# Optimization experiments

Hardware: AMD Instinct MI355X
Metric: run time of the kernel (lower is better)

## Reference

```python
import jax, jax.numpy as jnp
import numpy as np

N_NODES = 100000
N_EDGES = 1600000
IN_DIM = 64
HID = 64
EDGE_DIM = 1
NUM_GRAPHS = 1000
SCALE = 0.05


def setup_inputs() -> dict:
    key = jax.random.key(0)
    ks = jax.random.split(key, 20)
    x = jax.random.normal(ks[0], (N_NODES, IN_DIM), dtype=jnp.float32)
    edge_index = jax.random.randint(ks[1], (2, N_EDGES), 0, N_NODES, dtype=jnp.int64)
    edge_attr = jax.random.normal(ks[2], (N_EDGES, EDGE_DIM), dtype=jnp.float32)
    batch = jnp.sort(jax.random.randint(ks[3], (N_NODES,), 0, NUM_GRAPHS, dtype=jnp.int64))
    p = lambda k, shp: SCALE * jax.random.normal(k, shp, dtype=jnp.float32)
    return {
        "x": x, "edge_index": edge_index, "edge_attr": edge_attr, "batch": batch,
        # conv1 MLP + edge lin
        "W1a": p(ks[4], (IN_DIM, HID)), "b1a": p(ks[5], (HID,)),
        "W1b": p(ks[6], (HID, HID)), "b1b": p(ks[7], (HID,)),
        "We1": p(ks[8], (EDGE_DIM, IN_DIM)), "be1": p(ks[9], (IN_DIM,)),
        # conv2 MLP + edge lin
        "W2a": p(ks[10], (HID, HID)), "b2a": p(ks[11], (HID,)),
        "W2b": p(ks[12], (HID, HID)), "b2b": p(ks[13], (HID,)),
        "We2": p(ks[14], (EDGE_DIM, HID)), "be2": p(ks[15], (HID,)),
        # classifier
        "Wc1": p(ks[16], (HID, HID)), "bc1": p(ks[17], (HID,)),
        "Wc2": p(ks[18], (HID, 1)), "bc2": p(ks[19], (1,)),
    }


def _gine(x, src, dst, e_proj, Wa, ba, Wb, bb):
    # message: ReLU(x_src + projected edge feature); scatter-sum to target
    msg = jax.nn.relu(x[src] + e_proj)                      # [E, D]
    agg = jax.ops.segment_sum(msg, dst, num_segments=x.shape[0])
    h = x + agg                                             # eps = 0 (default)
    return jax.nn.relu(h @ Wa + ba) @ Wb + bb               # GIN MLP


def reference(x, edge_index, edge_attr, batch,
              W1a, b1a, W1b, b1b, We1, be1,
              W2a, b2a, W2b, b2b, We2, be2,
              Wc1, bc1, Wc2, bc2):
    src, dst = edge_index[0], edge_index[1]
    h = _gine(x, src, dst, edge_attr @ We1 + be1, W1a, b1a, W1b, b1b)
    h = jax.nn.relu(h)  # dropout is identity in eval mode
    h = _gine(h, src, dst, edge_attr @ We2 + be2, W2a, b2a, W2b, b2b)
    h = jax.nn.relu(h)
    # global mean pool over graphs
    sums = jax.ops.segment_sum(h, batch, num_segments=NUM_GRAPHS)
    cnts = jax.ops.segment_sum(jnp.ones((h.shape[0], 1), h.dtype), batch, num_segments=NUM_GRAPHS)
    pooled = sums / jnp.maximum(cnts, 1.0)                  # [G, HID]
    return jax.nn.relu(pooled @ Wc1 + bc1) @ Wc2 + bc2      # [G, 1]
```

## Files before the change

kernel.cpp:

```cpp
#include <hip/hip_runtime.h>

#define N_NODES    100000
#define N_EDGES    1600000
#define DIM        64
#define NUM_GRAPHS 1000
#define CONV_BLK   3125
#define PAD        72

#define SLICES     512
#define SLICE_E    3125
#define NBUCK      782
#define CAP4       3072

typedef __attribute__((ext_vector_type(8))) short bf16x8;
typedef __attribute__((ext_vector_type(4))) float f32x4;

__device__ __forceinline__ unsigned short f2bf(float f) {
    unsigned int b = __float_as_uint(f);
    b += 0x7FFFu + ((b >> 16) & 1u);
    return (unsigned short)(b >> 16);
}

__device__ __forceinline__ float4 ntload_f4(const float* p) {
    f32x4 v = __builtin_nontemporal_load((const f32x4*)p);
    return make_float4(v.x, v.y, v.z, v.w);
}

__global__ __launch_bounds__(256) void prep(
    const int* __restrict__ ei, const float* __restrict__ x,
    int* __restrict__ hist, int* __restrict__ bucketTotal,
    unsigned short* __restrict__ x16)
{
    __shared__ int lh[NBUCK];
    int blk = blockIdx.x, t = threadIdx.x;
    if (blk < SLICES) {
        for (int i = t; i < NBUCK; i += 256) lh[i] = 0;
        __syncthreads();
        const int* dsts = ei + N_EDGES + blk * SLICE_E;
        for (int k = t; k < SLICE_E; k += 256)
            atomicAdd(&lh[dsts[k] >> 7], 1);
        __syncthreads();
        for (int i = t; i < NBUCK; i += 256) {
            int h = lh[i];
            hist[blk * NBUCK + i] = h;
            if (h) atomicAdd(&bucketTotal[i], h);
        }
    } else {
        int tt = (blk - SLICES) * 256 + t;
        if (tt < N_NODES * DIM / 8) {
            int base = tt * 8;
            float4 f0 = ntload_f4(x + base);
            float4 f1 = ntload_f4(x + base + 4);
            uint4 o;
            o.x = (unsigned)f2bf(f0.x) | ((unsigned)f2bf(f0.y) << 16);
            o.y = (unsigned)f2bf(f0.z) | ((unsigned)f2bf(f0.w) << 16);
            o.z = (unsigned)f2bf(f1.x) | ((unsigned)f2bf(f1.y) << 16);
            o.w = (unsigned)f2bf(f1.z) | ((unsigned)f2bf(f1.w) << 16);
            *(uint4*)(x16 + base) = o;
        }
    }
}

__global__ __launch_bounds__(1024) void csr_c2a(
    const int* __restrict__ bucketTotal, int* __restrict__ bucketStart)
{
    __shared__ int sc[1024];
    int t = threadIdx.x;
    int v = (t < NBUCK) ? bucketTotal[t] : 0;
    sc[t] = v;
    __syncthreads();
    for (int o = 1; o < 1024; o <<= 1) {
        int u = (t >= o) ? sc[t - o] : 0;
        __syncthreads();
        sc[t] += u;
        __syncthreads();
    }
    if (t < NBUCK) bucketStart[t] = sc[t] - v;
    if (t == NBUCK - 1) bucketStart[NBUCK] = sc[t];
}

__global__ __launch_bounds__(512) void csr_c2b(
    const int* __restrict__ hist, const int* __restrict__ bucketStart,
    int* __restrict__ off)
{
    __shared__ int sc[512];
    int b = blockIdx.x, t = threadIdx.x;
    int v = hist[t * NBUCK + b];
    sc[t] = v;
    __syncthreads();
    for (int o = 1; o < 512; o <<= 1) {
        int u = (t >= o) ? sc[t - o] : 0;
        __syncthreads();
        sc[t] += u;
        __syncthreads();
    }
    off[b * SLICES + t] = bucketStart[b] + sc[t] - v;
}

__global__ __launch_bounds__(256) void csr_c3(
    const int* __restrict__ ei, const float* __restrict__ ea,
    const int* __restrict__ hist, const int* __restrict__ off,
    int2* __restrict__ tmp)
{
    __shared__ int2 staging[SLICE_E];
    __shared__ int  lstart[NBUCK + 1];
    __shared__ int  garr[NBUCK];
    __shared__ int  lcur[NBUCK];
    __shared__ unsigned short barr[SLICE_E];
    __shared__ int  part[256];

    int s = blockIdx.x, t = threadIdx.x;

    int h[4];
    int mysum = 0;
    #pragma unroll
    for (int j = 0; j < 4; ++j) {
        int b = 4 * t + j;
        h[j] = (b < NBUCK) ? hist[s * NBUCK + b] : 0;
        mysum += h[j];
    }
    part[t] = mysum;
    for (int i = t; i < NBUCK; i += 256) {
        garr[i] = off[i * SLICES + s];
        lcur[i] = 0;
    }
    __syncthreads();
    for (int o = 1; o < 256; o <<= 1) {
        int u = (t >= o) ? part[t - o] : 0;
        __syncthreads();
        part[t] += u;
        __syncthreads();
    }
    int run = part[t] - mysum;
    #pragma unroll
    for (int j = 0; j < 4; ++j) {
        int b = 4 * t + j;
        if (b < NBUCK) lstart[b] = run;
        run += h[j];
    }
    if (t == 0) lstart[NBUCK] = SLICE_E;
    __syncthreads();

    #pragma unroll
    for (int j = 0; j < 4; ++j) {
        int b = 4 * t + j;
        if (b < NBUCK)
            for (int i = lstart[b]; i < lstart[b + 1]; ++i)
                barr[i] = (unsigned short)b;
    }
    __syncthreads();

    for (int k = t; k < SLICE_E; k += 256) {
        int e   = s * SLICE_E + k;
        int src = ei[e];
        int dst = ei[N_EDGES + e];
        float a = ea[e];
        int b   = dst >> 7;
        int p   = lstart[b] + atomicAdd(&lcur[b], 1);
        staging[p] = make_int2(((dst & 127) << 17) | src, __float_as_int(a));
    }
    __syncthreads();

    for (int i = t; i < SLICE_E; i += 256) {
        int b = barr[i];
        tmp[garr[b] + (i - lstart[b])] = staging[i];
    }
}

__global__ __launch_bounds__(256) void csr_c4(
    const int2* __restrict__ tmp, const int* __restrict__ bucketStart,
    int2* __restrict__ csr_e, int* __restrict__ rowptr)
{
    __shared__ int2 staging[CAP4];
    __shared__ int  nh[128];
    __shared__ int  nscan[128];
    __shared__ int  ncur[128];

    int b = blockIdx.x, t = threadIdx.x;
    int lo = bucketStart[b], hi = bucketStart[b + 1];
    int cnt = hi - lo;
    int node0 = b << 7;
    int nn = min(128, N_NODES - node0);

    if (t < 128) { nh[t] = 0; ncur[t] = 0; }
    __syncthreads();

    int2 r[12];
    int nr = 0;
    for (int k = t; k < cnt; k += 256) {
        int2 v = tmp[lo + k];
        r[nr++] = v;
        atomicAdd(&nh[v.x >> 17], 1);
    }
    __syncthreads();

    if (t < 128) nscan[t] = nh[t];
    __syncthreads();
    for (int o = 1; o < 128; o <<= 1) {
        int u = (t >= o && t < 128) ? nscan[t - o] : 0;
        __syncthreads();
        if (t < 128) nscan[t] += u;
        __syncthreads();
    }
    if (t < 128) nscan[t] -= nh[t];
    __syncthreads();

    if (t < nn) rowptr[node0 + t] = lo + nscan[t];
    if (b == NBUCK - 1 && t == 0) rowptr[N_NODES] = N_EDGES;

    for (int k = 0; k < nr; ++k) {
        int dl = r[k].x >> 17;
        int p  = nscan[dl] + atomicAdd(&ncur[dl], 1);
        staging[p] = r[k];
    }
    __syncthreads();

    for (int i = t; i < cnt; i += 256) {
        int2 v = staging[i];
        csr_e[lo + i] = make_int2((v.x & 0x1FFFF) << 4, v.y);
    }
}

__global__ __launch_bounds__(128) void build_perm(
    const int* __restrict__ rowptr, int* __restrict__ perm)
{
    __shared__ unsigned skey[128];
    int b = blockIdx.x, t = threadIdx.x;
    int node0 = b << 7;
    int nn = min(128, N_NODES - node0);

    unsigned key = 0xFFFFFFFFu;
    if (t < nn) {
        int d = rowptr[node0 + t + 1] - rowptr[node0 + t];
        key = ((unsigned)d << 7) | (unsigned)t;
    }
    skey[t] = key;
    for (int k = 2; k <= 128; k <<= 1)
        for (int j = k >> 1; j > 0; j >>= 1) {
            __syncthreads();
            int ixj = t ^ j;
            if (ixj > t) {
                unsigned a = skey[t], c = skey[ixj];
                bool asc = ((t & k) == 0);
                if ((a > c) == asc) { skey[t] = c; skey[ixj] = a; }
            }
        }
    __syncthreads();
    if (t < nn) {
        unsigned e = skey[t];
        int nd = node0 + (int)(e & 127u);
        perm[node0 + t] = (int)(((e >> 7) << 17) | (unsigned)nd);
    }
}

template<bool SELF32>
__global__ __launch_bounds__(512, 8) void gine_mfma(
    const uint2* __restrict__ g2,
    const float* __restrict__ self32,
    const int*   __restrict__ rowptr,
    const int*   __restrict__ perm,
    const int2*  __restrict__ csr_e,
    const float* __restrict__ We, const float* __restrict__ be,
    const float* __restrict__ Wa, const float* __restrict__ ba,
    const float* __restrict__ Wb, const float* __restrict__ bb,
    unsigned int* __restrict__ out16)
{
    __shared__ short sWat[64 * PAD];
    __shared__ short sWbt[64 * PAD];
    __shared__ short h16[32 * PAD];
    __shared__ short t16[32 * PAD];

    int t = threadIdx.x;
    for (int i = t; i < 4096; i += 512) {
        int k = i >> 6, n = i & 63;
        sWat[n * PAD + k] = (short)f2bf(Wa[i]);
        sWbt[n * PAD + k] = (short)f2bf(Wb[i]);
    }
    int wave = t >> 6;
    int lane = t & 63;
    int quad = lane >> 4;
    int l15  = lane & 15;
    int slot = wave * 4 + quad;
    int d0   = l15 * 4;
    float4 wp = *(const float4*)(We + d0);
    float4 bp = *(const float4*)(be + d0);
    int mtile = wave & 1;
    int ntile = wave >> 1;
    int col   = ntile * 16 + l15;
    int am    = mtile * 16 + l15;
    float bav = ba[col], bbv = bb[col];
    __syncthreads();

    for (int base = blockIdx.x * 32; base < N_NODES; base += gridDim.x * 32) {
        int  pslot = base + slot;
        bool valid = pslot < N_NODES;
        int  pe   = valid ? perm[pslot] : 0;
        int  node = pe & 0x1FFFF;
        int  deg  = (int)((unsigned)pe >> 17);
        int  beg  = 0;
        if (valid) beg = min(rowptr[node], N_EDGES - 1);
        int dm = deg;
        dm = max(dm, __shfl_xor(dm, 16));
        dm = max(dm, __shfl_xor(dm, 32));

        float4 agg = make_float4(0.f, 0.f, 0.f, 0.f);
        #define EDGE4(rr, uu, cond)                                              \
        {                                                                        \
            float s = (cond) ? 1.f : 0.f, av = __int_as_float(rr.y);             \
            float e0 = __uint_as_float(uu.x << 16);                              \
            float e1 = __uint_as_float(uu.x & 0xFFFF0000u);                      \
            float e2 = __uint_as_float(uu.y << 16);                              \
            float e3 = __uint_as_float(uu.y & 0xFFFF0000u);                      \
            agg.x = fmaf(s, fmaxf(e0 + fmaf(av, wp.x, bp.x), 0.f), agg.x);       \
            agg.y = fmaf(s, fmaxf(e1 + fmaf(av, wp.y, bp.y), 0.f), agg.y);       \
            agg.z = fmaf(s, fmaxf(e2 + fmaf(av, wp.z, bp.z), 0.f), agg.z);       \
            agg.w = fmaf(s, fmaxf(e3 + fmaf(av, wp.w, bp.w), 0.f), agg.w);       \
        }
        for (int j = 0; j < dm; j += 4) {
            int2 r0 = csr_e[beg + ((j + 0) < deg ? j + 0 : 0)];
            int2 r1 = csr_e[beg + ((j + 1) < deg ? j + 1 : 0)];
            int2 r2 = csr_e[beg + ((j + 2) < deg ? j + 2 : 0)];
            int2 r3 = csr_e[beg + ((j + 3) < deg ? j + 3 : 0)];
            uint2 u0 = g2[r0.x + l15];
            uint2 u1 = g2[r1.x + l15];
            uint2 u2 = g2[r2.x + l15];
            uint2 u3 = g2[r3.x + l15];
            EDGE4(r0, u0, (j + 0) < deg)
            EDGE4(r1, u1, (j + 1) < deg)
            EDGE4(r2, u2, (j + 2) < deg)
            EDGE4(r3, u3, (j + 3) < deg)
        }
        #undef EDGE4
        if (valid) {
            if (SELF32) {
                float4 sv = *(const float4*)(self32 + (size_t)node * DIM + d0);
                agg.x += sv.x; agg.y += sv.y; agg.z += sv.z; agg.w += sv.w;
            } else {
                uint2 u = g2[node * 16 + l15];
                agg.x += __uint_as_float(u.x << 16);
                agg.y += __uint_as_float(u.x & 0xFFFF0000u);
                agg.z += __uint_as_float(u.y << 16);
                agg.w += __uint_as_float(u.y & 0xFFFF0000u);
            }
        }
        {
            unsigned lo = (unsigned)f2bf(agg.x) | ((unsigned)f2bf(agg.y) << 16);
            unsigned hi = (unsigned)f2bf(agg.z) | ((unsigned)f2bf(agg.w) << 16);
            *(uint2*)&h16[slot * PAD + d0] = make_uint2(lo, hi);
        }
        __syncthreads();

        f32x4 acc = {bav, bav, bav, bav};
        #pragma unroll
        for (int s = 0; s < 2; ++s) {
            bf16x8 a = *(const bf16x8*)&h16[am * PAD + s * 32 + quad * 8];
            bf16x8 b = *(const bf16x8*)&sWat[col * PAD + s * 32 + quad * 8];
            acc = __builtin_amdgcn_mfma_f32_16x16x32_bf16(a, b, acc, 0, 0, 0);
        }
        #pragma unroll
        for (int r = 0; r < 4; ++r) {
            int row = mtile * 16 + quad * 4 + r;
            t16[row * PAD + col] = (short)f2bf(fmaxf(acc[r], 0.f));
        }
        __syncthreads();

        f32x4 acc2 = {bbv, bbv, bbv, bbv};
        #pragma unroll
        for (int s = 0; s < 2; ++s) {
            bf16x8 a = *(const bf16x8*)&t16[am * PAD + s * 32 + quad * 8];
            bf16x8 b = *(const bf16x8*)&sWbt[col * PAD + s * 32 + quad * 8];
            acc2 = __builtin_amdgcn_mfma_f32_16x16x32_bf16(a, b, acc2, 0, 0, 0);
        }
        #pragma unroll
        for (int r = 0; r < 4; ++r) {
            int row = mtile * 16 + quad * 4 + r;
            h16[row * PAD + col] = (short)f2bf(fmaxf(acc2[r], 0.f));
        }
        __syncthreads();
        {
            int nn = t >> 4, dd = (t & 15) * 2;
            int ps = base + nn;
            if (ps < N_NODES) {
                int nd = perm[ps] & 0x1FFFF;
                uint2 v = *(const uint2*)&h16[nn * PAD + dd * 2];
                *(uint2*)&out16[(size_t)nd * 32 + dd] = v;
            }
        }
        __syncthreads();
    }
}

__device__ __forceinline__ int lbound(const int* __restrict__ a, int key) {
    int lo = 0, hi = N_NODES;
    while (lo < hi) {
        int mid = (lo + hi) >> 1;
        if (a[mid] < key) lo = mid + 1; else hi = mid;
    }
    return lo;
}

__global__ __launch_bounds__(256) void pool_cls(
    const unsigned int* __restrict__ B16b,
    const int* __restrict__ batch,
    const float* __restrict__ Wc1,  const float* __restrict__ bc1,
    const float* __restrict__ Wc2,  const float* __restrict__ bc2,
    float* __restrict__ out)
{
    __shared__ float sW[64 * 64];
    __shared__ float sp[4][64];

    int t = threadIdx.x;
    for (int i = t; i < 64 * 64; i += 256) sW[i] = Wc1[i];

    int nl   = t >> 6;
    int lane = t & 63;
    int g    = blockIdx.x * 4 + nl;

    int p = lane & 31, h = lane >> 5;
    if (g < NUM_GRAPHS) {
        int s = lbound(batch, g);
        int e = lbound(batch, g + 1);
        float2 sum = make_float2(0.f, 0.f);
        for (int i = s + h; i < e; i += 2) {
            unsigned u = B16b[(size_t)i * 32 + p];
            sum.x += __uint_as_float(u << 16);
            sum.y += __uint_as_float(u & 0xFFFF0000u);
        }
        sum.x += __shfl_xor(sum.x, 32);
        sum.y += __shfl_xor(sum.y, 32);
        if (h == 0) {
            float inv = 1.f / (float)max(e - s, 1);
            sp[nl][2 * p]     = sum.x * inv;
            sp[nl][2 * p + 1] = sum.y * inv;
        }
    } else if (h == 0) {
        sp[nl][2 * p] = 0.f;
        sp[nl][2 * p + 1] = 0.f;
    }
    __syncthreads();

    float acc = bc1[lane];
    #pragma unroll
    for (int k = 0; k < 64; ++k)
        acc = fmaf(sp[nl][k], sW[k * 64 + lane], acc);
    float tv = fmaxf(acc, 0.f) * Wc2[lane];

    #pragma unroll
    for (int off = 32; off > 0; off >>= 1)
        tv += __shfl_down(tv, off);

    if (lane == 0 && g < NUM_GRAPHS) out[g] = tv + bc2[0];
}

extern "C" void kernel_launch(void* const* d_in, const int* in_sizes, int n_in,
                              void* d_out, int out_size, void* d_ws, size_t ws_size,
                              hipStream_t stream) {
    const float* x     = (const float*)d_in[0];
    const int*   ei    = (const int*)  d_in[1];
    const float* ea    = (const float*)d_in[2];
    const int*   batch = (const int*)  d_in[3];
    const float* W1a = (const float*)d_in[4];
    const float* b1a = (const float*)d_in[5];
    const float* W1b = (const float*)d_in[6];
    const float* b1b = (const float*)d_in[7];
    const float* We1 = (const float*)d_in[8];
    const float* be1 = (const float*)d_in[9];
    const float* W2a = (const float*)d_in[10];
    const float* b2a = (const float*)d_in[11];
    const float* W2b = (const float*)d_in[12];
    const float* b2b = (const float*)d_in[13];
    const float* We2 = (const float*)d_in[14];
    const float* be2 = (const float*)d_in[15];
    const float* Wc1 = (const float*)d_in[16];
    const float* bc1 = (const float*)d_in[17];
    const float* Wc2 = (const float*)d_in[18];
    const float* bc2 = (const float*)d_in[19];

    int2*           csr_e  = (int2*)d_ws;
    unsigned short* x16    = (unsigned short*)(csr_e + N_EDGES);
    unsigned short* B16    = x16 + (size_t)N_NODES * DIM;
    unsigned short* B16b   = B16 + (size_t)N_NODES * DIM;
    int2*           tmp    = (int2*)B16b;
    int*            hist   = (int*)(B16b + (size_t)N_NODES * DIM);
    int*            off    = hist + SLICES * NBUCK;
    int*            bucketTotal = off + NBUCK * SLICES;
    int*            bucketStart = bucketTotal + NBUCK;
    int*            rowptr = bucketStart + (NBUCK + 1);
    int*            perm   = hist;

    hipMemsetAsync(bucketTotal, 0, NBUCK * sizeof(int), stream);

    prep<<<SLICES + CONV_BLK, 256, 0, stream>>>(ei, x, hist, bucketTotal, x16);
    csr_c2a<<<1, 1024, 0, stream>>>(bucketTotal, bucketStart);
    csr_c2b<<<NBUCK, 512, 0, stream>>>(hist, bucketStart, off);
    csr_c3<<<SLICES, 256, 0, stream>>>(ei, ea, hist, off, tmp);
    csr_c4<<<NBUCK, 256, 0, stream>>>(tmp, bucketStart, csr_e, rowptr);
    build_perm<<<NBUCK, 128, 0, stream>>>(rowptr, perm);

    gine_mfma<true><<<1024, 512, 0, stream>>>(
        (const uint2*)x16, x, rowptr, perm, csr_e,
        We1, be1, W1a, b1a, W1b, b1b, (unsigned int*)B16);

    gine_mfma<false><<<1024, 512, 0, stream>>>(
        (const uint2*)B16, nullptr, rowptr, perm, csr_e,
        We2, be2, W2a, b2a, W2b, b2b, (unsigned int*)B16b);

    pool_cls<<<(NUM_GRAPHS + 3) / 4, 256, 0, stream>>>(
        (const unsigned int*)B16b, batch, Wc1, bc1, Wc2, bc2, (float*)d_out);
}
```

Baseline: 308.6 us.

## Split fused GINE conv into separate aggregation and MLP kernels

Splits the fused per-node gather-and-MLP kernel into two kernels: a sync-free aggregation kernel with one node per 16-lane group that writes bf16 aggregates to a scratch buffer, and a 128-row MLP kernel that keeps weights in register MFMA fragments. This removes the four block-wide barriers per 32-node tile and the LDS weight staging from the latency-bound gather loop, so more waves can stay resident. In exchange it adds two extra kernel launches and a round trip of the aggregated features through global memory. The scratch buffer reuses the B16b region, which the second layer's output later overwrites after the MLP has read it.

Result: slower. 337.8 us (+9.5%).

```diff
diff --git a/kernel.cpp b/kernel.cpp
--- a/kernel.cpp
+++ b/kernel.cpp
@@ -254,45 +254,27 @@
 }
 
 template<bool SELF32>
-__global__ __launch_bounds__(512, 8) void gine_mfma(
+__global__ __launch_bounds__(256, 8) void gine_agg(
     const uint2* __restrict__ g2,
     const float* __restrict__ self32,
     const int*   __restrict__ rowptr,
     const int*   __restrict__ perm,
     const int2*  __restrict__ csr_e,
     const float* __restrict__ We, const float* __restrict__ be,
-    const float* __restrict__ Wa, const float* __restrict__ ba,
-    const float* __restrict__ Wb, const float* __restrict__ bb,
-    unsigned int* __restrict__ out16)
-{
-    __shared__ short sWat[64 * PAD];
-    __shared__ short sWbt[64 * PAD];
-    __shared__ short h16[32 * PAD];
-    __shared__ short t16[32 * PAD];
-
+    uint2* __restrict__ hout)
+{
     int t = threadIdx.x;
-    for (int i = t; i < 4096; i += 512) {
-        int k = i >> 6, n = i & 63;
-        sWat[n * PAD + k] = (short)f2bf(Wa[i]);
-        sWbt[n * PAD + k] = (short)f2bf(Wb[i]);
-    }
     int wave = t >> 6;
     int lane = t & 63;
     int quad = lane >> 4;
     int l15  = lane & 15;
-    int slot = wave * 4 + quad;
     int d0   = l15 * 4;
     float4 wp = *(const float4*)(We + d0);
     float4 bp = *(const float4*)(be + d0);
-    int mtile = wave & 1;
-    int ntile = wave >> 1;
-    int col   = ntile * 16 + l15;
-    int am    = mtile * 16 + l15;
-    float bav = ba[col], bbv = bb[col];
-    __syncthreads();
-
-    for (int base = blockIdx.x * 32; base < N_NODES; base += gridDim.x * 32) {
-        int  pslot = base + slot;
+
+    int stride = gridDim.x * 16;
+    for (int base = blockIdx.x * 16 + wave * 4; base < N_NODES; base += stride) {
+        int  pslot = base + quad;
         bool valid = pslot < N_NODES;
         int  pe   = valid ? perm[pslot] : 0;
         int  node = pe & 0x1FFFF;
@@ -342,51 +324,71 @@
                 agg.z += __uint_as_float(u.y << 16);
                 agg.w += __uint_as_float(u.y & 0xFFFF0000u);
             }
-        }
-        {
             unsigned lo = (unsigned)f2bf(agg.x) | ((unsigned)f2bf(agg.y) << 16);
             unsigned hi = (unsigned)f2bf(agg.z) | ((unsigned)f2bf(agg.w) << 16);
-            *(uint2*)&h16[slot * PAD + d0] = make_uint2(lo, hi);
-        }
-        __syncthreads();
-
+            hout[node * 16 + l15] = make_uint2(lo, hi);
+        }
+    }
+}
+
+__global__ __launch_bounds__(512, 8) void mlp128(
+    const unsigned short* __restrict__ hin,
+    const float* __restrict__ Wa, const float* __restrict__ ba,
+    const float* __restrict__ Wb, const float* __restrict__ bb,
+    unsigned short* __restrict__ hout)
+{
+    __shared__ short t16[128 * PAD];
+
+    int t = threadIdx.x;
+    int wave = t >> 6, lane = t & 63, quad = lane >> 4, l15 = lane & 15;
+    int ntile = wave >> 1;
+    int mhalf = wave & 1;
+    int col = ntile * 16 + l15;
+
+    bf16x8 fragA[2], fragB[2];
+    #pragma unroll
+    for (int s = 0; s < 2; ++s) {
+        #pragma unroll
+        for (int j = 0; j < 8; ++j) {
+            int k = s * 32 + quad * 8 + j;
+            fragA[s][j] = (short)f2bf(Wa[k * 64 + col]);
+            fragB[s][j] = (short)f2bf(Wb[k * 64 + col]);
+        }
+    }
+    float bav = ba[col], bbv = bb[col];
+    int node0 = blockIdx.x << 7;
+
+    #pragma unroll
+    for (int mt = 0; mt < 4; ++mt) {
+        int rbase = mhalf * 64 + mt * 16;
+        int row = min(node0 + rbase + l15, N_NODES - 1);
         f32x4 acc = {bav, bav, bav, bav};
         #pragma unroll
         for (int s = 0; s < 2; ++s) {
-            bf16x8 a = *(const bf16x8*)&h16[am * PAD + s * 32 + quad * 8];
-            bf16x8 b = *(const bf16x8*)&sWat[col * PAD + s * 32 + quad * 8];
-            acc = __builtin_amdgcn_mfma_f32_16x16x32_bf16(a, b, acc, 0, 0, 0);
+            bf16x8 a = *(const bf16x8*)&hin[(size_t)row * DIM + s * 32 + quad * 8];
+            acc = __builtin_amdgcn_mfma_f32_16x16x32_bf16(a, fragA[s], acc, 0, 0, 0);
+        }
+        #pragma unroll
+        for (int r = 0; r < 4; ++r)
+            t16[(rbase + quad * 4 + r) * PAD + col] = (short)f2bf(fmaxf(acc[r], 0.f));
+    }
+    __syncthreads();
+
+    #pragma unroll
+    for (int mt = 0; mt < 4; ++mt) {
+        int rbase = mhalf * 64 + mt * 16;
+        f32x4 acc = {bbv, bbv, bbv, bbv};
+        #pragma unroll
+        for (int s = 0; s < 2; ++s) {
+            bf16x8 a = *(const bf16x8*)&t16[(rbase + l15) * PAD + s * 32 + quad * 8];
+            acc = __builtin_amdgcn_mfma_f32_16x16x32_bf16(a, fragB[s], acc, 0, 0, 0);
         }
         #pragma unroll
         for (int r = 0; r < 4; ++r) {
-            int row = mtile * 16 + quad * 4 + r;
-            t16[row * PAD + col] = (short)f2bf(fmaxf(acc[r], 0.f));
-        }
-        __syncthreads();
-
-        f32x4 acc2 = {bbv, bbv, bbv, bbv};
-        #pragma unroll
-        for (int s = 0; s < 2; ++s) {
-            bf16x8 a = *(const bf16x8*)&t16[am * PAD + s * 32 + quad * 8];
-            bf16x8 b = *(const bf16x8*)&sWbt[col * PAD + s * 32 + quad * 8];
-            acc2 = __builtin_amdgcn_mfma_f32_16x16x32_bf16(a, b, acc2, 0, 0, 0);
-        }
-        #pragma unroll
-        for (int r = 0; r < 4; ++r) {
-            int row = mtile * 16 + quad * 4 + r;
-            h16[row * PAD + col] = (short)f2bf(fmaxf(acc2[r], 0.f));
-        }
-        __syncthreads();
-        {
-            int nn = t >> 4, dd = (t & 15) * 2;
-            int ps = base + nn;
-            if (ps < N_NODES) {
-                int nd = perm[ps] & 0x1FFFF;
-                uint2 v = *(const uint2*)&h16[nn * PAD + dd * 2];
-                *(uint2*)&out16[(size_t)nd * 32 + dd] = v;
-            }
-        }
-        __syncthreads();
+            int row = node0 + rbase + quad * 4 + r;
+            if (row < N_NODES)
+                hout[(size_t)row * DIM + col] = (unsigned short)f2bf(fmaxf(acc[r], 0.f));
+        }
     }
 }
 
@@ -481,6 +483,7 @@
     unsigned short* B16    = x16 + (size_t)N_NODES * DIM;
     unsigned short* B16b   = B16 + (size_t)N_NODES * DIM;
     int2*           tmp    = (int2*)B16b;
+    unsigned short* hbuf   = B16b;
     int*            hist   = (int*)(B16b + (size_t)N_NODES * DIM);
     int*            off    = hist + SLICES * NBUCK;
     int*            bucketTotal = off + NBUCK * SLICES;
@@ -497,13 +500,15 @@
     csr_c4<<<NBUCK, 256, 0, stream>>>(tmp, bucketStart, csr_e, rowptr);
     build_perm<<<NBUCK, 128, 0, stream>>>(rowptr, perm);
 
-    gine_mfma<true><<<1024, 512, 0, stream>>>(
+    gine_agg<true><<<6250, 256, 0, stream>>>(
         (const uint2*)x16, x, rowptr, perm, csr_e,
-        We1, be1, W1a, b1a, W1b, b1b, (unsigned int*)B16);
-
-    gine_mfma<false><<<1024, 512, 0, stream>>>(
+        We1, be1, (uint2*)hbuf);
+    mlp128<<<NBUCK, 512, 0, stream>>>(hbuf, W1a, b1a, W1b, b1b, B16);
+
+    gine_agg<false><<<6250, 256, 0, stream>>>(
         (const uint2*)B16, nullptr, rowptr, perm, csr_e,
-        We2, be2, W2a, b2a, W2b, b2b, (unsigned int*)B16b);
+        We2, be2, (uint2*)hbuf);
+    mlp128<<<NBUCK, 512, 0, stream>>>(hbuf, W2a, b2a, W2b, b2b, B16b);
 
     pool_cls<<<(NUM_GRAPHS + 3) / 4, 256, 0, stream>>>(
         (const unsigned int*)B16b, batch, Wc1, bc1, Wc2, bc2, (float*)d_out);
```

## Replace two-pass bucket sort CSR build with atomic degree count and scatter

Applied to the files above, without the earlier changes.

The CSR construction drops the slice-histogram, two-level bucket sort (c2b, c3, c4) and instead counts per-node degree with global atomics, scans degrees per 128-node block, then scatters each edge to its position via an atomic cursor per destination. This removes several kernels and the staging buffer traffic. In exchange, edge order within a row becomes nondeterministic, so float summation order varies between runs, and there are many global atomics on random addresses.

After: 434.6 us. 1.41x slower.

```diff
diff --git a/kernel.cpp b/kernel.cpp
--- a/kernel.cpp
+++ b/kernel.cpp
@@ -5,12 +5,9 @@
 #define DIM        64
 #define NUM_GRAPHS 1000
 #define CONV_BLK   3125
+#define DEG_BLK    1563
 #define PAD        72
-
-#define SLICES     512
-#define SLICE_E    3125
 #define NBUCK      782
-#define CAP4       3072
 
 typedef __attribute__((ext_vector_type(8))) short bf16x8;
 typedef __attribute__((ext_vector_type(4))) float f32x4;
@@ -28,25 +25,20 @@
 
 __global__ __launch_bounds__(256) void prep(
     const int* __restrict__ ei, const float* __restrict__ x,
-    int* __restrict__ hist, int* __restrict__ bucketTotal,
-    unsigned short* __restrict__ x16)
-{
-    __shared__ int lh[NBUCK];
+    int* __restrict__ deg, unsigned short* __restrict__ x16)
+{
     int blk = blockIdx.x, t = threadIdx.x;
-    if (blk < SLICES) {
-        for (int i = t; i < NBUCK; i += 256) lh[i] = 0;
-        __syncthreads();
-        const int* dsts = ei + N_EDGES + blk * SLICE_E;
-        for (int k = t; k < SLICE_E; k += 256)
-            atomicAdd(&lh[dsts[k] >> 7], 1);
-        __syncthreads();
-        for (int i = t; i < NBUCK; i += 256) {
-            int h = lh[i];
-            hist[blk * NBUCK + i] = h;
-            if (h) atomicAdd(&bucketTotal[i], h);
+    if (blk < DEG_BLK) {
+        int e4 = blk * 256 + t;
+        if (e4 < N_EDGES / 4) {
+            int4 d = *(const int4*)(ei + N_EDGES + e4 * 4);
+            atomicAdd(&deg[d.x], 1);
+            atomicAdd(&deg[d.y], 1);
+            atomicAdd(&deg[d.z], 1);
+            atomicAdd(&deg[d.w], 1);
         }
     } else {
-        int tt = (blk - SLICES) * 256 + t;
+        int tt = (blk - DEG_BLK) * 256 + t;
         if (tt < N_NODES * DIM / 8) {
             int base = tt * 8;
             float4 f0 = ntload_f4(x + base);
@@ -61,6 +53,26 @@
     }
 }
 
+__global__ __launch_bounds__(128) void csr_s1(
+    const int* __restrict__ deg, int* __restrict__ rowptr,
+    int* __restrict__ bucketTotal)
+{
+    __shared__ int sc[128];
+    int b = blockIdx.x, t = threadIdx.x;
+    int node = (b << 7) + t;
+    int d = (node < N_NODES) ? deg[node] : 0;
+    sc[t] = d;
+    __syncthreads();
+    for (int o = 1; o < 128; o <<= 1) {
+        int u = (t >= o) ? sc[t - o] : 0;
+        __syncthreads();
+        sc[t] += u;
+        __syncthreads();
+    }
+    if (node < N_NODES) rowptr[node] = sc[t] - d;
+    if (t == 0) bucketTotal[b] = sc[127];
+}
+
 __global__ __launch_bounds__(1024) void csr_c2a(
     const int* __restrict__ bucketTotal, int* __restrict__ bucketStart)
 {
@@ -79,161 +91,26 @@
     if (t == NBUCK - 1) bucketStart[NBUCK] = sc[t];
 }
 
-__global__ __launch_bounds__(512) void csr_c2b(
-    const int* __restrict__ hist, const int* __restrict__ bucketStart,
-    int* __restrict__ off)
-{
-    __shared__ int sc[512];
-    int b = blockIdx.x, t = threadIdx.x;
-    int v = hist[t * NBUCK + b];
-    sc[t] = v;
-    __syncthreads();
-    for (int o = 1; o < 512; o <<= 1) {
-        int u = (t >= o) ? sc[t - o] : 0;
-        __syncthreads();
-        sc[t] += u;
-        __syncthreads();
-    }
-    off[b * SLICES + t] = bucketStart[b] + sc[t] - v;
-}
-
-__global__ __launch_bounds__(256) void csr_c3(
-    const int* __restrict__ ei, const float* __restrict__ ea,
-    const int* __restrict__ hist, const int* __restrict__ off,
-    int2* __restrict__ tmp)
-{
-    __shared__ int2 staging[SLICE_E];
-    __shared__ int  lstart[NBUCK + 1];
-    __shared__ int  garr[NBUCK];
-    __shared__ int  lcur[NBUCK];
-    __shared__ unsigned short barr[SLICE_E];
-    __shared__ int  part[256];
-
-    int s = blockIdx.x, t = threadIdx.x;
-
-    int h[4];
-    int mysum = 0;
-    #pragma unroll
-    for (int j = 0; j < 4; ++j) {
-        int b = 4 * t + j;
-        h[j] = (b < NBUCK) ? hist[s * NBUCK + b] : 0;
-        mysum += h[j];
-    }
-    part[t] = mysum;
-    for (int i = t; i < NBUCK; i += 256) {
-        garr[i] = off[i * SLICES + s];
-        lcur[i] = 0;
-    }
-    __syncthreads();
-    for (int o = 1; o < 256; o <<= 1) {
-        int u = (t >= o) ? part[t - o] : 0;
-        __syncthreads();
-        part[t] += u;
-        __syncthreads();
-    }
-    int run = part[t] - mysum;
-    #pragma unroll
-    for (int j = 0; j < 4; ++j) {
-        int b = 4 * t + j;
-        if (b < NBUCK) lstart[b] = run;
-        run += h[j];
-    }
-    if (t == 0) lstart[NBUCK] = SLICE_E;
-    __syncthreads();
-
-    #pragma unroll
-    for (int j = 0; j < 4; ++j) {
-        int b = 4 * t + j;
-        if (b < NBUCK)
-            for (int i = lstart[b]; i < lstart[b + 1]; ++i)
-                barr[i] = (unsigned short)b;
-    }
-    __syncthreads();
-
-    for (int k = t; k < SLICE_E; k += 256) {
-        int e   = s * SLICE_E + k;
-        int src = ei[e];
-        int dst = ei[N_EDGES + e];
-        float a = ea[e];
-        int b   = dst >> 7;
-        int p   = lstart[b] + atomicAdd(&lcur[b], 1);
-        staging[p] = make_int2(((dst & 127) << 17) | src, __float_as_int(a));
-    }
-    __syncthreads();
-
-    for (int i = t; i < SLICE_E; i += 256) {
-        int b = barr[i];
-        tmp[garr[b] + (i - lstart[b])] = staging[i];
-    }
-}
-
-__global__ __launch_bounds__(256) void csr_c4(
-    const int2* __restrict__ tmp, const int* __restrict__ bucketStart,
-    int2* __restrict__ csr_e, int* __restrict__ rowptr)
-{
-    __shared__ int2 staging[CAP4];
-    __shared__ int  nh[128];
-    __shared__ int  nscan[128];
-    __shared__ int  ncur[128];
-
-    int b = blockIdx.x, t = threadIdx.x;
-    int lo = bucketStart[b], hi = bucketStart[b + 1];
-    int cnt = hi - lo;
-    int node0 = b << 7;
-    int nn = min(128, N_NODES - node0);
-
-    if (t < 128) { nh[t] = 0; ncur[t] = 0; }
-    __syncthreads();
-
-    int2 r[12];
-    int nr = 0;
-    for (int k = t; k < cnt; k += 256) {
-        int2 v = tmp[lo + k];
-        r[nr++] = v;
-        atomicAdd(&nh[v.x >> 17], 1);
-    }
-    __syncthreads();
-
-    if (t < 128) nscan[t] = nh[t];
-    __syncthreads();
-    for (int o = 1; o < 128; o <<= 1) {
-        int u = (t >= o && t < 128) ? nscan[t - o] : 0;
-        __syncthreads();
-        if (t < 128) nscan[t] += u;
-        __syncthreads();
-    }
-    if (t < 128) nscan[t] -= nh[t];
-    __syncthreads();
-
-    if (t < nn) rowptr[node0 + t] = lo + nscan[t];
-    if (b == NBUCK - 1 && t == 0) rowptr[N_NODES] = N_EDGES;
-
-    for (int k = 0; k < nr; ++k) {
-        int dl = r[k].x >> 17;
-        int p  = nscan[dl] + atomicAdd(&ncur[dl], 1);
-        staging[p] = r[k];
-    }
-    __syncthreads();
-
-    for (int i = t; i < cnt; i += 256) {
-        int2 v = staging[i];
-        csr_e[lo + i] = make_int2((v.x & 0x1FFFF) << 4, v.y);
-    }
-}
-
-__global__ __launch_bounds__(128) void build_perm(
-    const int* __restrict__ rowptr, int* __restrict__ perm)
+__global__ __launch_bounds__(128) void csr_s3(
+    const int* __restrict__ deg, const int* __restrict__ bucketStart,
+    int* __restrict__ rowptr, int* __restrict__ cursor,
+    int* __restrict__ perm)
 {
     __shared__ unsigned skey[128];
     int b = blockIdx.x, t = threadIdx.x;
     int node0 = b << 7;
+    int node = node0 + t;
     int nn = min(128, N_NODES - node0);
 
     unsigned key = 0xFFFFFFFFu;
     if (t < nn) {
-        int d = rowptr[node0 + t + 1] - rowptr[node0 + t];
-        key = ((unsigned)d << 7) | (unsigned)t;
-    }
+        int r = rowptr[node] + bucketStart[b];
+        rowptr[node] = r;
+        cursor[node] = r;
+        key = ((unsigned)deg[node] << 7) | (unsigned)t;
+    }
+    if (b == NBUCK - 1 && t == 0) rowptr[N_NODES] = bucketStart[NBUCK];
+
     skey[t] = key;
     for (int k = 2; k <= 128; k <<= 1)
         for (int j = k >> 1; j > 0; j >>= 1) {
@@ -251,6 +128,18 @@
         int nd = node0 + (int)(e & 127u);
         perm[node0 + t] = (int)(((e >> 7) << 17) | (unsigned)nd);
     }
+}
+
+__global__ __launch_bounds__(256) void csr_scatter(
+    const int* __restrict__ ei, const float* __restrict__ ea,
+    int* __restrict__ cursor, int2* __restrict__ csr_e)
+{
+    int e = blockIdx.x * 256 + threadIdx.x;
+    int src = ei[e];
+    int dst = ei[N_EDGES + e];
+    float a = ea[e];
+    int p = atomicAdd(&cursor[dst], 1);
+    csr_e[p] = make_int2(src << 4, __float_as_int(a));
 }
 
 template<bool SELF32>
@@ -480,22 +369,20 @@
     unsigned short* x16    = (unsigned short*)(csr_e + N_EDGES);
     unsigned short* B16    = x16 + (size_t)N_NODES * DIM;
     unsigned short* B16b   = B16 + (size_t)N_NODES * DIM;
-    int2*           tmp    = (int2*)B16b;
-    int*            hist   = (int*)(B16b + (size_t)N_NODES * DIM);
-    int*            off    = hist + SLICES * NBUCK;
-    int*            bucketTotal = off + NBUCK * SLICES;
+    int*            deg    = (int*)(B16b + (size_t)N_NODES * DIM);
+    int*            rowptr = deg + N_NODES;
+    int*            cursor = rowptr + N_NODES + 1;
+    int*            perm   = cursor + N_NODES;
+    int*            bucketTotal = perm + N_NODES;
     int*            bucketStart = bucketTotal + NBUCK;
-    int*            rowptr = bucketStart + (NBUCK + 1);
-    int*            perm   = hist;
-
-    hipMemsetAsync(bucketTotal, 0, NBUCK * sizeof(int), stream);
-
-    prep<<<SLICES + CONV_BLK, 256, 0, stream>>>(ei, x, hist, bucketTotal, x16);
+
+    hipMemsetAsync(deg, 0, N_NODES * sizeof(int), stream);
+
+    prep<<<DEG_BLK + CONV_BLK, 256, 0, stream>>>(ei, x, deg, x16);
+    csr_s1<<<NBUCK, 128, 0, stream>>>(deg, rowptr, bucketTotal);
     csr_c2a<<<1, 1024, 0, stream>>>(bucketTotal, bucketStart);
-    csr_c2b<<<NBUCK, 512, 0, stream>>>(hist, bucketStart, off);
-    csr_c3<<<SLICES, 256, 0, stream>>>(ei, ea, hist, off, tmp);
-    csr_c4<<<NBUCK, 256, 0, stream>>>(tmp, bucketStart, csr_e, rowptr);
-    build_perm<<<NBUCK, 128, 0, stream>>>(rowptr, perm);
+    csr_s3<<<NBUCK, 128, 0, stream>>>(deg, bucketStart, rowptr, cursor, perm);
+    csr_scatter<<<N_EDGES / 256, 256, 0, stream>>>(ei, ea, cursor, csr_e);
 
     gine_mfma<true><<<1024, 512, 0, stream>>>(
         (const uint2*)x16, x, rowptr, perm, csr_e,
```
